# Optimization experiments

Hardware: AMD Instinct MI355X
Metric: run time of the kernel (lower is better)

The kernel has to match this reference:

```python
import jax, jax.numpy as jnp
import numpy as np

sigmoid = jax.nn.sigmoid

def lstm_layer(x_seq, W, U, b, act):
    """Keras-style LSTM. x_seq: [B,T,D], W: [D,4H], U: [H,4H], b: [4H].
    Gate order i,f,c,o. recurrent_activation=sigmoid, cell/output activation=act.
    Returns full hidden sequence [B,T,H]."""
    B, T, D = x_seq.shape
    H = U.shape[0]
    # precompute input contribution for all timesteps: [T,B,4H]
    xW = jnp.einsum('btd,dg->tbg', x_seq, W) + b
    h0 = jnp.zeros((B, H), x_seq.dtype)
    c0 = jnp.zeros((B, H), x_seq.dtype)

    def step(carry, xw_t):
        h, c = carry
        z = xw_t + h @ U  # [B,4H]
        i, f, g, o = jnp.split(z, 4, axis=-1)
        i = sigmoid(i)
        f = sigmoid(f)
        g = act(g)
        o = sigmoid(o)
        c_new = f * c + i * g
        h_new = o * act(c_new)
        return (h_new, c_new), h_new

    (_, _), hs = jax.lax.scan(step, (h0, c0), xW)  # hs: [T,B,H]
    return jnp.transpose(hs, (1, 0, 2))


def setup_inputs() -> dict:
    key = jax.random.key(0)
    ks = jax.random.split(key, 7)
    B, T, V, E, H1, H2 = 4096, 200, 30000, 32, 32, 1
    x = jax.random.randint(ks[0], (B, T), 0, V, dtype=jnp.int32)
    emb = jax.random.normal(ks[1], (V, E), jnp.float32) * 0.05
    W1 = jax.random.normal(ks[2], (E, 4 * H1), jnp.float32) * 0.1
    U1 = jax.random.normal(ks[3], (H1, 4 * H1), jnp.float32) * 0.1
    b1 = jnp.zeros((4 * H1,), jnp.float32)
    W2 = jax.random.normal(ks[4], (H1, 4 * H2), jnp.float32) * 0.1
    U2 = jax.random.normal(ks[5], (H2, 4 * H2), jnp.float32) * 0.1
    b2 = jnp.zeros((4 * H2,), jnp.float32)
    return {"x": x, "emb": emb, "W1": W1, "U1": U1, "b1": b1,
            "W2": W2, "U2": U2, "b2": b2}


def reference(x, emb, W1, U1, b1, W2, U2, b2):
    e = emb[x]                                   # [B,T,32] embedding lookup
    h1 = lstm_layer(e, W1, U1, b1, jnp.tanh)     # [B,T,32]
    h2 = lstm_layer(h1, W2, U2, b2, sigmoid)     # [B,T,1] (activation='sigmoid')
    return h2[:, -1, :]                          # return_sequences=False -> last step [B,1]
```

## Files before the change

### kernel.cpp

```cpp
#include <hip/hip_runtime.h>
#include <hip/hip_bf16.h>

#define DEV_INLINE __device__ __forceinline__

typedef float v2f __attribute__((ext_vector_type(2)));
typedef __fp16 h2v __attribute__((ext_vector_type(2)));

DEV_INLINE int rl_i(int v, int l) { return __builtin_amdgcn_readlane(v, l); }
DEV_INLINE float rlf(float v, int l) {
    return __uint_as_float(__builtin_amdgcn_readlane(__float_as_uint(v), l));
}
DEV_INLINE float sigmoid_f(float x) { return __builtin_amdgcn_rcpf(1.0f + __expf(-x)); }

#if __has_builtin(__builtin_amdgcn_fdot2)
DEV_INLINE float fdot2(h2v a, h2v b, float c) { return __builtin_amdgcn_fdot2(a, b, c, false); }
#else
DEV_INLINE float fdot2(h2v a, h2v b, float c) {
    return fmaf((float)a[0], (float)b[0], fmaf((float)a[1], (float)b[1], c));
}
#endif

DEV_INLINE float dpp_swap1(float v) {
    int r = __builtin_amdgcn_update_dpp(__float_as_int(v), __float_as_int(v),
                                        0xB1, 0xF, 0xF, false);
    return __int_as_float(r);
}

DEV_INLINE void bcast_halves(float v, bool low, float& lo_b, float& hi_b) {
#if __has_builtin(__builtin_amdgcn_permlane32_swap)
    auto r = __builtin_amdgcn_permlane32_swap(__float_as_uint(v), __float_as_uint(v),
                                              false, false);
    lo_b = __uint_as_float(r[0]);
    hi_b = __uint_as_float(r[1]);
#else
    float vx = __shfl_xor(v, 32);
    lo_b = low ? v : vx;
    hi_b = low ? vx : v;
#endif
}

__global__ __launch_bounds__(128) void embw_kernel(
    const float* __restrict__ emb, const float* __restrict__ W1,
    const float* __restrict__ b1, float* __restrict__ embW)
{
    const int v = blockIdx.x, c = threadIdx.x;
    __shared__ float e[32];
    if (c < 32) e[c] = emb[v * 32 + c];
    __syncthreads();
    float acc = b1[c];
#pragma unroll
    for (int d = 0; d < 32; ++d) acc = fmaf(e[d], W1[d * 128 + c], acc);
    embW[v * 128 + ((c & 63) << 1) + (c >> 6)] = acc;
}

template<int MODE>
__global__ __launch_bounds__(256) void lstm_kernel(
    const int* __restrict__ x, const float* __restrict__ embW,
    const float* __restrict__ emb, const float* __restrict__ W1,
    const float* __restrict__ b1, const float* __restrict__ U1,
    const float* __restrict__ W2, const float* __restrict__ U2,
    const float* __restrict__ b2, float* __restrict__ out, int T)
{
    const int lane = threadIdx.x & 63;
    const int wave = threadIdx.x >> 6;
    const int b    = blockIdx.x * 4 + wave;
    const bool low = lane < 32;
    const int ca = lane, cb = lane + 64;

    h2v upa[16], upb[16];
#pragma unroll
    for (int m = 0; m < 16; ++m) {
        h2v ta, tb;
        ta[0] = (__fp16)U1[(2 * m) * 128 + ca];
        ta[1] = (__fp16)U1[(2 * m + 1) * 128 + ca];
        tb[0] = (__fp16)U1[(2 * m) * 128 + cb];
        tb[1] = (__fp16)U1[(2 * m + 1) * 128 + cb];
        upa[m] = ta; upb[m] = tb;
    }

    h2v wpa[16], wpb[16];
    float ba = 0.f, bb = 0.f;
    if constexpr (MODE == 1) {
#pragma unroll
        for (int m = 0; m < 16; ++m) {
            h2v ta, tb;
            ta[0] = (__fp16)W1[(2 * m) * 128 + ca];
            ta[1] = (__fp16)W1[(2 * m + 1) * 128 + ca];
            tb[0] = (__fp16)W1[(2 * m) * 128 + cb];
            tb[1] = (__fp16)W1[(2 * m + 1) * 128 + cb];
            wpa[m] = ta; wpb[m] = tb;
        }
        ba = b1[ca]; bb = b1[cb];
    }

    const int gsel = lane >> 4;
    h2v w2p[16];
#pragma unroll
    for (int m = 0; m < 16; ++m) {
        h2v tw;
        tw[0] = (__fp16)W2[(2 * m) * 4 + gsel];
        tw[1] = (__fp16)W2[(2 * m + 1) * 4 + gsel];
        w2p[m] = tw;
    }
    const float u2s = U2[gsel];
    const float b2s = b2[gsel];

    const int* xrow = x + b * T;

    float h = 0.f, c = 0.f, h2 = 0.f, c2 = 0.f;
    int hp[16];

#define LAYER2_UPDATE()                                                        \
    do {                                                                       \
        float p0 = 0.f, p1 = 0.f;                                              \
        _Pragma("unroll")                                                      \
        for (int m = 0; m < 16; m += 2) {                                      \
            p0 = fdot2(__builtin_bit_cast(h2v, hp[m]),     w2p[m],     p0);    \
            p1 = fdot2(__builtin_bit_cast(h2v, hp[m + 1]), w2p[m + 1], p1);    \
        }                                                                      \
        float s2 = sigmoid_f((p0 + p1) + fmaf(u2s, h2, b2s));                  \
        float i2 = rlf(s2, 0),  f2 = rlf(s2, 16);                              \
        float g2 = rlf(s2, 32), o2 = rlf(s2, 48);                              \
        c2 = fmaf(f2, c2, i2 * g2);                                            \
        h2 = o2 * sigmoid_f(c2);                                               \
    } while (0)

    int idxA = __builtin_amdgcn_readfirstlane(xrow[0]);
    int idxB = __builtin_amdgcn_readfirstlane(xrow[1]);

    v2f zc;
    float ec[32];
    if constexpr (MODE == 0) {
        zc = reinterpret_cast<const v2f*>(embW)[idxA * 64 + lane];
    } else {
#pragma unroll
        for (int d = 0; d < 32; ++d) ec[d] = emb[idxA * 32 + d];
    }

#pragma unroll 2
    for (int t = 0; t < T; ++t) {
        v2f zn;
        float en[32];
        if constexpr (MODE == 0) {
            zn = reinterpret_cast<const v2f*>(embW)[idxB * 64 + lane];
        } else {
#pragma unroll
            for (int d = 0; d < 32; ++d) en[d] = emb[idxB * 32 + d];
        }
        idxB = __builtin_amdgcn_readfirstlane(xrow[(t + 2 < T) ? (t + 2) : (T - 1)]);

        float hx = dpp_swap1(h);
        int hpi = __builtin_bit_cast(int, __builtin_amdgcn_cvt_pkrtz(h, hx));
#pragma unroll
        for (int m = 0; m < 16; ++m) hp[m] = rl_i(hpi, 2 * m);

        float za0, zb0;
        if constexpr (MODE == 0) {
            za0 = zc.x; zb0 = zc.y;
        } else {
            za0 = ba; zb0 = bb;
#pragma unroll
            for (int m = 0; m < 16; ++m) {
                h2v ep = __builtin_amdgcn_cvt_pkrtz(ec[2 * m], ec[2 * m + 1]);
                za0 = fdot2(ep, wpa[m], za0);
                zb0 = fdot2(ep, wpb[m], zb0);
            }
        }
        float za1 = 0.f, zb1 = 0.f;
#pragma unroll
        for (int m = 0; m < 16; m += 2) {
            h2v h0 = __builtin_bit_cast(h2v, hp[m]);
            h2v h1 = __builtin_bit_cast(h2v, hp[m + 1]);
            za0 = fdot2(h0, upa[m],     za0);
            zb0 = fdot2(h0, upb[m],     zb0);
            za1 = fdot2(h1, upa[m + 1], za1);
            zb1 = fdot2(h1, upb[m + 1], zb1);
        }
        const float za = za0 + za1;
        const float zb = zb0 + zb1;

        if (t) LAYER2_UPDATE();

        float sa = sigmoid_f(za);
        float xb_ = low ? 2.0f * zb : zb;
        float u  = sigmoid_f(xb_);
        float rb = low ? 2.0f * u - 1.0f : u;

        float iv, fv, gv, ov;
        bcast_halves(sa, low, iv, fv);
        bcast_halves(rb, low, gv, ov);

        c = fmaf(fv, c, iv * gv);
        float tc = 2.0f * sigmoid_f(2.0f * c) - 1.0f;
        h = ov * tc;

        if constexpr (MODE == 0) {
            zc = zn;
        } else {
#pragma unroll
            for (int d = 0; d < 32; ++d) ec[d] = en[d];
        }
    }

    {
        float hx = dpp_swap1(h);
        int hpi = __builtin_bit_cast(int, __builtin_amdgcn_cvt_pkrtz(h, hx));
#pragma unroll
        for (int m = 0; m < 16; ++m) hp[m] = rl_i(hpi, 2 * m);
        LAYER2_UPDATE();
    }

    if (lane == 0) out[b] = h2;
#undef LAYER2_UPDATE
}

extern "C" void kernel_launch(void* const* d_in, const int* in_sizes, int n_in,
                              void* d_out, int out_size, void* d_ws, size_t ws_size,
                              hipStream_t stream) {
    const int*   x   = (const int*)d_in[0];
    const float* emb = (const float*)d_in[1];
    const float* W1  = (const float*)d_in[2];
    const float* U1  = (const float*)d_in[3];
    const float* b1  = (const float*)d_in[4];
    const float* W2  = (const float*)d_in[5];
    const float* U2  = (const float*)d_in[6];
    const float* b2  = (const float*)d_in[7];
    float* out = (float*)d_out;

    const int V = in_sizes[1] / 32;
    const int T = 200;
    const int B = in_sizes[0] / T;
    const int blocks = B / 4;

    const size_t need = (size_t)V * 128 * sizeof(float);
    if (ws_size >= need) {
        float* embW = (float*)d_ws;
        embw_kernel<<<V, 128, 0, stream>>>(emb, W1, b1, embW);
        lstm_kernel<0><<<blocks, 256, 0, stream>>>(x, embW, emb, W1, b1, U1,
                                                   W2, U2, b2, out, T);
    } else {
        lstm_kernel<1><<<blocks, 256, 0, stream>>>(x, nullptr, emb, W1, b1, U1,
                                                   W2, U2, b2, out, T);
    }
}
```

Measured before the change: 293.3 us.

## Split each batch row's LSTM across two waves with LDS gate exchange

Each batch element now runs on a 128-thread block of two waves, one gate column per lane, instead of one wave doing two columns per lane. Gate activations and the fp16 hidden state are exchanged through shared memory with two barriers per timestep. Layer 2 now runs on the second wave as a DPP row reduction. The embW precompute is also restructured to stage W1 in LDS and handle 16 vocab rows per block, and the input prefetch is one step deeper. This halves the per-lane recurrent dot-product work and raises parallelism, but adds barrier and LDS round-trip latency to the serial dependency chain of every step.

```diff
diff --git a/kernel.cpp b/kernel.cpp
--- a/kernel.cpp
+++ b/kernel.cpp
@@ -6,10 +6,10 @@
 typedef float v2f __attribute__((ext_vector_type(2)));
 typedef __fp16 h2v __attribute__((ext_vector_type(2)));
 
-DEV_INLINE int rl_i(int v, int l) { return __builtin_amdgcn_readlane(v, l); }
 DEV_INLINE float rlf(float v, int l) {
     return __uint_as_float(__builtin_amdgcn_readlane(__float_as_uint(v), l));
 }
+DEV_INLINE int rfl(int v) { return __builtin_amdgcn_readfirstlane(v); }
 DEV_INLINE float sigmoid_f(float x) { return __builtin_amdgcn_rcpf(1.0f + __expf(-x)); }
 
 #if __has_builtin(__builtin_amdgcn_fdot2)
@@ -20,10 +20,16 @@
 }
 #endif
 
-DEV_INLINE float dpp_swap1(float v) {
-    int r = __builtin_amdgcn_update_dpp(__float_as_int(v), __float_as_int(v),
-                                        0xB1, 0xF, 0xF, false);
-    return __int_as_float(r);
+DEV_INLINE void lds_barrier() {
+    asm volatile("s_waitcnt lgkmcnt(0)" ::: "memory");
+    __builtin_amdgcn_s_barrier();
+    asm volatile("" ::: "memory");
+}
+
+template<int N>
+DEV_INLINE float ror_add(float v) {
+    int r = __builtin_amdgcn_update_dpp(0, __float_as_int(v), 0x120 + N, 0xF, 0xF, true);
+    return v + __int_as_float(r);
 }
 
 DEV_INLINE void bcast_halves(float v, bool low, float& lo_b, float& hi_b) {
@@ -39,22 +45,34 @@
 #endif
 }
 
-__global__ __launch_bounds__(128) void embw_kernel(
+__global__ __launch_bounds__(256) void embw_kernel(
     const float* __restrict__ emb, const float* __restrict__ W1,
     const float* __restrict__ b1, float* __restrict__ embW)
 {
-    const int v = blockIdx.x, c = threadIdx.x;
-    __shared__ float e[32];
-    if (c < 32) e[c] = emb[v * 32 + c];
+    __shared__ float w[4096];
+    const int tid = threadIdx.x;
+#pragma unroll
+    for (int i = 0; i < 16; ++i) w[tid + i * 256] = W1[tid + i * 256];
     __syncthreads();
-    float acc = b1[c];
-#pragma unroll
-    for (int d = 0; d < 32; ++d) acc = fmaf(e[d], W1[d * 128 + c], acc);
-    embW[v * 128 + ((c & 63) << 1) + (c >> 6)] = acc;
+
+    const int c   = tid & 127;
+    const int sub = tid >> 7;
+    const float bc = b1[c];
+    const int v0 = blockIdx.x * 16;
+
+#pragma unroll
+    for (int r = sub; r < 16; r += 2) {
+        const int v = v0 + r;
+        const float* e = emb + (size_t)v * 32;
+        float acc = bc;
+#pragma unroll
+        for (int d = 0; d < 32; ++d) acc = fmaf(e[d], w[d * 128 + c], acc);
+        embW[(size_t)v * 128 + c] = acc;
+    }
 }
 
 template<int MODE>
-__global__ __launch_bounds__(256) void lstm_kernel(
+__global__ __launch_bounds__(128, 8) void lstm_kernel(
     const int* __restrict__ x, const float* __restrict__ embW,
     const float* __restrict__ emb, const float* __restrict__ W1,
     const float* __restrict__ b1, const float* __restrict__ U1,
@@ -62,156 +80,148 @@
     const float* __restrict__ b2, float* __restrict__ out, int T)
 {
     const int lane = threadIdx.x & 63;
-    const int wave = threadIdx.x >> 6;
-    const int b    = blockIdx.x * 4 + wave;
+    const int wv   = threadIdx.x >> 6;
+    const int b    = blockIdx.x;
     const bool low = lane < 32;
-    const int ca = lane, cb = lane + 64;
-
-    h2v upa[16], upb[16];
+    const int col  = wv * 64 + lane;
+
+    h2v up[16];
 #pragma unroll
     for (int m = 0; m < 16; ++m) {
-        h2v ta, tb;
-        ta[0] = (__fp16)U1[(2 * m) * 128 + ca];
-        ta[1] = (__fp16)U1[(2 * m + 1) * 128 + ca];
-        tb[0] = (__fp16)U1[(2 * m) * 128 + cb];
-        tb[1] = (__fp16)U1[(2 * m + 1) * 128 + cb];
-        upa[m] = ta; upb[m] = tb;
-    }
-
-    h2v wpa[16], wpb[16];
-    float ba = 0.f, bb = 0.f;
+        h2v t;
+        t[0] = (__fp16)U1[(2 * m) * 128 + col];
+        t[1] = (__fp16)U1[(2 * m + 1) * 128 + col];
+        up[m] = t;
+    }
+
+    h2v wp[16]; float bcol = 0.f;
     if constexpr (MODE == 1) {
 #pragma unroll
         for (int m = 0; m < 16; ++m) {
-            h2v ta, tb;
-            ta[0] = (__fp16)W1[(2 * m) * 128 + ca];
-            ta[1] = (__fp16)W1[(2 * m + 1) * 128 + ca];
-            tb[0] = (__fp16)W1[(2 * m) * 128 + cb];
-            tb[1] = (__fp16)W1[(2 * m + 1) * 128 + cb];
-            wpa[m] = ta; wpb[m] = tb;
-        }
-        ba = b1[ca]; bb = b1[cb];
+            h2v t;
+            t[0] = (__fp16)W1[(2 * m) * 128 + col];
+            t[1] = (__fp16)W1[(2 * m + 1) * 128 + col];
+            wp[m] = t;
+        }
+        bcol = b1[col];
     }
 
     const int gsel = lane >> 4;
-    h2v w2p[16];
-#pragma unroll
-    for (int m = 0; m < 16; ++m) {
-        h2v tw;
-        tw[0] = (__fp16)W2[(2 * m) * 4 + gsel];
-        tw[1] = (__fp16)W2[(2 * m + 1) * 4 + gsel];
-        w2p[m] = tw;
-    }
+    const int pm   = lane & 15;
+    h2v w2s;
+    w2s[0] = (__fp16)W2[(2 * pm) * 4 + gsel];
+    w2s[1] = (__fp16)W2[(2 * pm + 1) * 4 + gsel];
     const float u2s = U2[gsel];
     const float b2s = b2[gsel];
 
+    __shared__ v2f gbuf[2][32];
+    __shared__ __align__(16) __fp16 hbuf[32];
+
     const int* xrow = x + b * T;
 
     float h = 0.f, c = 0.f, h2 = 0.f, c2 = 0.f;
-    int hp[16];
-
-#define LAYER2_UPDATE()                                                        \
-    do {                                                                       \
-        float p0 = 0.f, p1 = 0.f;                                              \
-        _Pragma("unroll")                                                      \
-        for (int m = 0; m < 16; m += 2) {                                      \
-            p0 = fdot2(__builtin_bit_cast(h2v, hp[m]),     w2p[m],     p0);    \
-            p1 = fdot2(__builtin_bit_cast(h2v, hp[m + 1]), w2p[m + 1], p1);    \
-        }                                                                      \
-        float s2 = sigmoid_f((p0 + p1) + fmaf(u2s, h2, b2s));                  \
-        float i2 = rlf(s2, 0),  f2 = rlf(s2, 16);                              \
-        float g2 = rlf(s2, 32), o2 = rlf(s2, 48);                              \
-        c2 = fmaf(f2, c2, i2 * g2);                                            \
-        h2 = o2 * sigmoid_f(c2);                                               \
-    } while (0)
-
-    int idxA = __builtin_amdgcn_readfirstlane(xrow[0]);
-    int idxB = __builtin_amdgcn_readfirstlane(xrow[1]);
-
-    v2f zc;
-    float ec[32];
+    h2v hp[16];
+#pragma unroll
+    for (int m = 0; m < 16; ++m) hp[m] = __builtin_bit_cast(h2v, 0);
+
+    int idxA = rfl(xrow[0]);
+    int idxB = rfl(xrow[1]);
+    int idxC = rfl(xrow[2]);
+
+    float zc = 0.f, zn = 0.f;
     if constexpr (MODE == 0) {
-        zc = reinterpret_cast<const v2f*>(embW)[idxA * 64 + lane];
-    } else {
-#pragma unroll
-        for (int d = 0; d < 32; ++d) ec[d] = emb[idxA * 32 + d];
+        zc = embW[(size_t)idxA * 128 + col];
+        zn = embW[(size_t)idxB * 128 + col];
     }
 
 #pragma unroll 2
     for (int t = 0; t < T; ++t) {
-        v2f zn;
-        float en[32];
+        float zf = 0.f;
+        if constexpr (MODE == 0) zf = embW[(size_t)idxC * 128 + col];
+        int idxN = rfl(xrow[(t + 3 < T) ? (t + 3) : (T - 1)]);
+
+        float a0, a1 = 0.f, a2 = 0.f, a3 = 0.f;
         if constexpr (MODE == 0) {
-            zn = reinterpret_cast<const v2f*>(embW)[idxB * 64 + lane];
+            a0 = zc;
         } else {
-#pragma unroll
-            for (int d = 0; d < 32; ++d) en[d] = emb[idxB * 32 + d];
-        }
-        idxB = __builtin_amdgcn_readfirstlane(xrow[(t + 2 < T) ? (t + 2) : (T - 1)]);
-
-        float hx = dpp_swap1(h);
-        int hpi = __builtin_bit_cast(int, __builtin_amdgcn_cvt_pkrtz(h, hx));
-#pragma unroll
-        for (int m = 0; m < 16; ++m) hp[m] = rl_i(hpi, 2 * m);
-
-        float za0, zb0;
-        if constexpr (MODE == 0) {
-            za0 = zc.x; zb0 = zc.y;
+            a0 = bcol;
+            const v2f* e2 = reinterpret_cast<const v2f*>(emb + (size_t)idxA * 32);
+#pragma unroll
+            for (int m = 0; m < 16; m += 2) {
+                v2f ea = e2[m], eb = e2[m + 1];
+                a0 = fdot2(__builtin_amdgcn_cvt_pkrtz(ea.x, ea.y), wp[m],     a0);
+                a1 = fdot2(__builtin_amdgcn_cvt_pkrtz(eb.x, eb.y), wp[m + 1], a1);
+            }
+        }
+#pragma unroll
+        for (int m = 0; m < 16; m += 4) {
+            a0 = fdot2(hp[m],     up[m],     a0);
+            a1 = fdot2(hp[m + 1], up[m + 1], a1);
+            a2 = fdot2(hp[m + 2], up[m + 2], a2);
+            a3 = fdot2(hp[m + 3], up[m + 3], a3);
+        }
+        const float z = (a0 + a1) + (a2 + a3);
+
+        float iv, fv, gv, ov;
+        if (wv == 0) {
+            float sa = sigmoid_f(z);
+            bcast_halves(sa, low, iv, fv);
+            if (low) gbuf[0][lane] = (v2f){iv, fv};
         } else {
-            za0 = ba; zb0 = bb;
-#pragma unroll
-            for (int m = 0; m < 16; ++m) {
-                h2v ep = __builtin_amdgcn_cvt_pkrtz(ec[2 * m], ec[2 * m + 1]);
-                za0 = fdot2(ep, wpa[m], za0);
-                zb0 = fdot2(ep, wpb[m], zb0);
-            }
-        }
-        float za1 = 0.f, zb1 = 0.f;
-#pragma unroll
-        for (int m = 0; m < 16; m += 2) {
-            h2v h0 = __builtin_bit_cast(h2v, hp[m]);
-            h2v h1 = __builtin_bit_cast(h2v, hp[m + 1]);
-            za0 = fdot2(h0, upa[m],     za0);
-            zb0 = fdot2(h0, upb[m],     zb0);
-            za1 = fdot2(h1, upa[m + 1], za1);
-            zb1 = fdot2(h1, upb[m + 1], zb1);
-        }
-        const float za = za0 + za1;
-        const float zb = zb0 + zb1;
-
-        if (t) LAYER2_UPDATE();
-
-        float sa = sigmoid_f(za);
-        float xb_ = low ? 2.0f * zb : zb;
-        float u  = sigmoid_f(xb_);
-        float rb = low ? 2.0f * u - 1.0f : u;
-
-        float iv, fv, gv, ov;
-        bcast_halves(sa, low, iv, fv);
-        bcast_halves(rb, low, gv, ov);
+            float xb = low ? 2.0f * z : z;
+            float u  = sigmoid_f(xb);
+            float rb = low ? 2.0f * u - 1.0f : u;
+            bcast_halves(rb, low, gv, ov);
+            if (low) gbuf[1][lane] = (v2f){gv, ov};
+        }
+        lds_barrier();
+
+        {
+            v2f other = gbuf[wv ^ 1][lane & 31];
+            if (wv == 0) { gv = other.x; ov = other.y; }
+            else         { iv = other.x; fv = other.y; }
+        }
 
         c = fmaf(fv, c, iv * gv);
         float tc = 2.0f * sigmoid_f(2.0f * c) - 1.0f;
         h = ov * tc;
 
-        if constexpr (MODE == 0) {
-            zc = zn;
-        } else {
-#pragma unroll
-            for (int d = 0; d < 32; ++d) ec[d] = en[d];
-        }
-    }
-
-    {
-        float hx = dpp_swap1(h);
-        int hpi = __builtin_bit_cast(int, __builtin_amdgcn_cvt_pkrtz(h, hx));
-#pragma unroll
-        for (int m = 0; m < 16; ++m) hp[m] = rl_i(hpi, 2 * m);
-        LAYER2_UPDATE();
-    }
-
-    if (lane == 0) out[b] = h2;
-#undef LAYER2_UPDATE
+        if (wv == 0 && low) hbuf[lane] = (__fp16)h;
+        lds_barrier();
+
+        {
+            const int4* hb4 = reinterpret_cast<const int4*>(hbuf);
+            int4 q0 = hb4[0], q1 = hb4[1], q2 = hb4[2], q3 = hb4[3];
+            hp[0]  = __builtin_bit_cast(h2v, q0.x); hp[1]  = __builtin_bit_cast(h2v, q0.y);
+            hp[2]  = __builtin_bit_cast(h2v, q0.z); hp[3]  = __builtin_bit_cast(h2v, q0.w);
+            hp[4]  = __builtin_bit_cast(h2v, q1.x); hp[5]  = __builtin_bit_cast(h2v, q1.y);
+            hp[6]  = __builtin_bit_cast(h2v, q1.z); hp[7]  = __builtin_bit_cast(h2v, q1.w);
+            hp[8]  = __builtin_bit_cast(h2v, q2.x); hp[9]  = __builtin_bit_cast(h2v, q2.y);
+            hp[10] = __builtin_bit_cast(h2v, q2.z); hp[11] = __builtin_bit_cast(h2v, q2.w);
+            hp[12] = __builtin_bit_cast(h2v, q3.x); hp[13] = __builtin_bit_cast(h2v, q3.y);
+            hp[14] = __builtin_bit_cast(h2v, q3.z); hp[15] = __builtin_bit_cast(h2v, q3.w);
+        }
+
+        if (wv == 1) {
+            const int* hbi = reinterpret_cast<const int*>(hbuf);
+            h2v php = __builtin_bit_cast(h2v, hbi[pm]);
+            float p = fdot2(php, w2s, 0.f);
+            p = ror_add<8>(p);
+            p = ror_add<4>(p);
+            p = ror_add<2>(p);
+            p = ror_add<1>(p);
+            float s2 = sigmoid_f(p + fmaf(u2s, h2, b2s));
+            float i2 = rlf(s2, 0),  f2 = rlf(s2, 16);
+            float g2 = rlf(s2, 32), o2 = rlf(s2, 48);
+            c2 = fmaf(f2, c2, i2 * g2);
+            h2 = o2 * sigmoid_f(c2);
+        }
+
+        zc = zn; zn = zf;
+        idxA = idxB; idxB = idxC; idxC = idxN;
+    }
+
+    if (wv == 1 && lane == 0) out[b] = h2;
 }
 
 extern "C" void kernel_launch(void* const* d_in, const int* in_sizes, int n_in,
@@ -230,16 +240,15 @@
     const int V = in_sizes[1] / 32;
     const int T = 200;
     const int B = in_sizes[0] / T;
-    const int blocks = B / 4;
 
     const size_t need = (size_t)V * 128 * sizeof(float);
     if (ws_size >= need) {
         float* embW = (float*)d_ws;
-        embw_kernel<<<V, 128, 0, stream>>>(emb, W1, b1, embW);
-        lstm_kernel<0><<<blocks, 256, 0, stream>>>(x, embW, emb, W1, b1, U1,
-                                                   W2, U2, b2, out, T);
+        embw_kernel<<<V / 16, 256, 0, stream>>>(emb, W1, b1, embW);
+        lstm_kernel<0><<<B, 128, 0, stream>>>(x, embW, emb, W1, b1, U1,
+                                              W2, U2, b2, out, T);
     } else {
-        lstm_kernel<1><<<blocks, 256, 0, stream>>>(x, nullptr, emb, W1, b1, U1,
-                                                   W2, U2, b2, out, T);
-    }
-}
+        lstm_kernel<1><<<B, 128, 0, stream>>>(x, nullptr, emb, W1, b1, U1,
+                                              W2, U2, b2, out, T);
+    }
+}
```

Result: no change. 295.7 us (+0.8%).
